# Performance work log

Hardware: AMD Instinct MI355X
Metric: run time of the kernel (lower is better)

## Reference

```python
import jax, jax.numpy as jnp
import numpy as np

N = 100_000          # nodes
E = 3_200_000        # edges (avg degree 32)
H = 20               # hidden_channels (node feature width, = 10 one-hot + 10 mlp)
EH = 64              # edge_hidden_dim
EO = 10              # edge_output_dim
THRESHOLD = 1.0


def setup_inputs() -> dict:
    key = jax.random.key(0)
    ks = jax.random.split(key, 12)
    x = jax.random.normal(ks[0], (N, 2, H), dtype=jnp.float32)
    edge_index = jax.random.randint(ks[1], (2, E), 0, N, dtype=jnp.int32)
    # distances strictly in (0, threshold]
    edge_attr = jax.random.uniform(ks[2], (E, 1), jnp.float32, 1e-4, THRESHOLD)
    # parameters (torch.rand init as in the module)
    a = jax.random.uniform(ks[3], (1,), jnp.float32)
    b = jax.random.uniform(ks[4], (1,), jnp.float32) + 1.0
    gamma1 = jax.random.uniform(ks[5], (H, H), jnp.float32)
    gamma2 = jax.random.uniform(ks[6], (H, H), jnp.float32)
    bias = jax.random.uniform(ks[7], (H,), jnp.float32)
    # edge MLP: Linear(1, EH) -> ReLU -> Linear(EH, EO)
    W1 = jax.random.normal(ks[8], (1, EH), jnp.float32)
    b1 = jnp.zeros((EH,), jnp.float32)
    W2 = jax.random.normal(ks[9], (EH, EO), jnp.float32) / np.sqrt(EH)
    b2 = jnp.zeros((EO,), jnp.float32)
    return dict(x=x, edge_index=edge_index, edge_attr=edge_attr, a=a, b=b,
                gamma1=gamma1, gamma2=gamma2, bias=bias, W1=W1, b1=b1, W2=W2, b2=b2)


def reference(x, edge_index, edge_attr, a, b, gamma1, gamma2, bias, W1, b1, W2, b2):
    src, dst = edge_index[0], edge_index[1]
    # --- edge features ---
    h = jax.nn.relu(edge_attr @ W1 + b1)            # [E, EH]
    mlp_out = h @ W2 + b2                           # [E, EO]
    # one-hot distance bucket: 10 equal intervals over (0, threshold], idx 10 -> 9
    idx = jnp.clip((edge_attr[:, 0] * (10.0 / THRESHOLD)).astype(jnp.int32), 0, 9)
    one_hot = jax.nn.one_hot(idx, 10, dtype=x.dtype)  # [E, 10]
    eac = jnp.concatenate([one_hot, mlp_out], axis=1)  # edge_attr_combined [E, 20]
    # --- per-source-node normalization (w_tilde) ---
    sum_w = jax.ops.segment_sum(eac, src, num_segments=N)  # [N, 20]
    sw = sum_w[src]                                        # [E, 20]
    safe = jnp.where(sw != 0, sw, 1.0)
    w_tilde = jnp.where(sw != 0, eac / safe, jnp.asarray(0.01, x.dtype))
    # --- rho weighting on node features ---
    h_j = x[src, 0]                                  # [E, 20]
    h_jp = x[dst, 0]                                 # [E, 20]
    rho = jnp.abs(a * h_j - (1.0 - a) * h_jp) ** b   # [E, 20]
    # --- aggregate messages per source node ---
    sum_features = jax.ops.segment_sum(rho * w_tilde, src, num_segments=N)  # [N, 20]
    # --- node update ---
    out0 = jax.nn.sigmoid(x[:, 0] @ gamma1.T + sum_features @ gamma2.T + bias)
    return jnp.stack([out0, sum_features], axis=1)   # [N, 2, 20]
```

## Files before the change

### kernel.cpp

```cpp
#include <hip/hip_runtime.h>
#include <hip/hip_bf16.h>


#define BATCH 4096
#define BPT   16
#define BSH   7
#define CAP   4608

__device__ int block_scan_excl(int* data, int n, int* scratch) {
    const int t = threadIdx.x;
    const int lane = t & 63, w = t >> 6;
    const int base = t * 4;
    int v0 = (base + 0 < n) ? data[base + 0] : 0;
    int v1 = (base + 1 < n) ? data[base + 1] : 0;
    int v2 = (base + 2 < n) ? data[base + 2] : 0;
    int v3 = (base + 3 < n) ? data[base + 3] : 0;
    int p1 = v0 + v1, p2 = p1 + v2, p3 = p2 + v3;
    int x = p3;
    #pragma unroll
    for (int o = 1; o < 64; o <<= 1) { int y = __shfl_up(x, o); if (lane >= o) x += y; }
    if (lane == 63) scratch[w] = x;
    __syncthreads();
    int wbase = 0;
    for (int i = 0; i < w; ++i) wbase += scratch[i];
    int tb = wbase + x - p3;
    if (base + 0 < n) data[base + 0] = tb;
    if (base + 1 < n) data[base + 1] = tb + v0;
    if (base + 2 < n) data[base + 2] = tb + p1;
    if (base + 3 < n) data[base + 3] = tb + p2;
    int tot = scratch[0] + scratch[1] + scratch[2] + scratch[3];
    __syncthreads();
    return tot;
}

__launch_bounds__(256)
__global__ void k_scatter(const int* __restrict__ src, const int* __restrict__ dst,
                          const float* __restrict__ ea, int* __restrict__ gcursor,
                          int* __restrict__ tmpw, unsigned char* __restrict__ tmpn,
                          const float* __restrict__ x, __hip_bfloat16* __restrict__ xa,
                          const float* __restrict__ W1, const float* __restrict__ b1,
                          const float* __restrict__ W2, const float* __restrict__ b2,
                          float* __restrict__ AB, int* __restrict__ flag,
                          int E, int nb, int Npack, int EH, int EO) {
    __shared__ int  pay[BATCH];
    __shared__ unsigned char pbn[BATCH];
    __shared__ unsigned short sbid[BATCH];
    __shared__ int  lcount[1024];
    __shared__ int  lsave[1024];
    __shared__ int  scratch[4];
    const int t = threadIdx.x;

    if (blockIdx.x == 0) {
        if (t == 64) {
            int ok = 1;
            for (int k = 0; k < EH; ++k) if (b1[k] != 0.0f) ok = 0;
            *flag = ok;
        }
        if (t < EO) {
            float A = 0.0f;
            for (int k = 0; k < EH; ++k)
                if (W1[k] > 0.0f) A = fmaf(W1[k], W2[k * EO + t], A);
            AB[t]      = A;
            AB[EO + t] = b2[t];
        }
    }

    for (int i = t; i < 1024; i += 256) lcount[i] = 0;
    __syncthreads();
    const int base = blockIdx.x * BATCH;
    int mys[BPT], myr[BPT], myw[BPT];
    #pragma unroll
    for (int k = 0; k < BPT; ++k) {
        int e = base + k * 256 + t;
        mys[k] = -1;
        if (e < E) {
            int s = src[e], d = dst[e];
            float dd = ea[e];
            int ib = (int)(dd * 10.0f);
            ib = ib < 0 ? 0 : (ib > 9 ? 9 : ib);
            int dq = (int)fmaf(dd, 2047.0f, 0.5f);
            dq = dq < 0 ? 0 : (dq > 2047 ? 2047 : dq);
            mys[k] = s;
            myr[k] = atomicAdd(&lcount[s >> BSH], 1);
            myw[k] = (d & 0x1FFFF) | (ib << 17) | (dq << 21);
        }
    }
    __syncthreads();
    for (int i = t; i < 1024; i += 256) lsave[i] = lcount[i];
    __syncthreads();
    int total = block_scan_excl(lcount, nb, scratch);
    for (int b = t; b < nb; b += 256) {
        int c = lsave[b];
        if (c > 0) lsave[b] = atomicAdd(&gcursor[b], c);
    }
    __syncthreads();
    #pragma unroll
    for (int k = 0; k < BPT; ++k) {
        if (mys[k] >= 0) {
            int b = mys[k] >> BSH;
            int pos = lcount[b] + myr[k];
            pay[pos]  = myw[k];
            pbn[pos]  = (unsigned char)(mys[k] & 127);
            sbid[pos] = (unsigned short)b;
        }
    }
    __syncthreads();
    for (int j = t; j < total; j += 256) {
        int b = sbid[j];
        int pos = lsave[b] + (j - lcount[b]);
        if (pos < CAP) {
            tmpw[b * CAP + pos] = pay[j];
            tmpn[b * CAP + pos] = pbn[j];
        }
    }
    const int stride = gridDim.x * 256;
    for (int i = blockIdx.x * 256 + t; i < Npack * 20; i += stride) {
        int n = i / 20, c = i - n * 20;
        xa[(n << 5) + c] = __float2bfloat16(x[n * 40 + c]);
    }
}

template <int USE_XA>
__launch_bounds__(512, 8)
__global__ void k_nodeb(const float* __restrict__ x,
                        const __hip_bfloat16* __restrict__ xa,
                        const int* __restrict__ gcount,
                        const int* __restrict__ tmpw,
                        const unsigned char* __restrict__ tmpn,
                        const float* __restrict__ a_p, const float* __restrict__ b_p,
                        const float* __restrict__ g1, const float* __restrict__ g2,
                        const float* __restrict__ bias,
                        const float* __restrict__ AB, const int* __restrict__ flag_p,
                        const float* __restrict__ W1, const float* __restrict__ b1,
                        const float* __restrict__ W2, const float* __restrict__ b2,
                        float* __restrict__ out, int N, int EH, int EO) {
    __shared__ int   buf[CAP];
    __shared__ int   hist[128];
    __shared__ int   rowstart[129];
    __shared__ int   lcur[128];
    __shared__ unsigned char perm[128];
    __shared__ __hip_bfloat16 s_x0[128 * 22];
    __shared__ float s_sf[128 * 21];
    __shared__ float s_g1[20 * 21], s_g2[20 * 21], s_b[20];

    const int t = threadIdx.x;
    const int b = blockIdx.x;
    const int node0 = b << BSH;
    const int s0 = b * CAP;
    int m = gcount[b];
    if (m > CAP) m = CAP;

    if (t < 128) hist[t] = 0;
    for (int i = t; i < 400; i += 512) {
        int r = i / 20, cc = i - r * 20;
        s_g1[r * 21 + cc] = g1[i];
        s_g2[r * 21 + cc] = g2[i];
    }
    if (t < 20) s_b[t] = bias[t];
    for (int i = t; i < 2560; i += 512) {
        int l = i / 20, cc = i - l * 20;
        int n = node0 + l;
        if (USE_XA)
            s_x0[l * 22 + cc] = (n < N) ? xa[(n << 5) + cc] : __float2bfloat16(0.0f);
        else
            s_x0[l * 22 + cc] = __float2bfloat16((n < N) ? x[n * 40 + cc] : 0.0f);
    }
    __syncthreads();

    const int4*   tw4 = (const int4*)(tmpw + s0);
    const uchar4* tn4 = (const uchar4*)(tmpn + s0);
    int vw[12], vn[12];
    #pragma unroll
    for (int k = 0; k < 3; ++k) {
        int idx4 = k * 512 + t;
        #pragma unroll
        for (int j = 0; j < 4; ++j) vn[k * 4 + j] = -1;
        int e0 = idx4 << 2;
        if (e0 < m) {
            int4   wv = tw4[idx4];
            uchar4 nv = tn4[idx4];
            vw[k * 4 + 0] = wv.x; vw[k * 4 + 1] = wv.y;
            vw[k * 4 + 2] = wv.z; vw[k * 4 + 3] = wv.w;
            { vn[k * 4 + 0] = nv.x & 127; atomicAdd(&hist[vn[k * 4 + 0]], 1); }
            if (e0 + 1 < m) { vn[k * 4 + 1] = nv.y & 127; atomicAdd(&hist[vn[k * 4 + 1]], 1); }
            if (e0 + 2 < m) { vn[k * 4 + 2] = nv.z & 127; atomicAdd(&hist[vn[k * 4 + 2]], 1); }
            if (e0 + 3 < m) { vn[k * 4 + 3] = nv.w & 127; atomicAdd(&hist[vn[k * 4 + 3]], 1); }
        }
    }
    __syncthreads();
    if (t < 64) {
        int a = hist[2 * t], bb = hist[2 * t + 1];
        int s = a + bb;
        int xsc = s;
        #pragma unroll
        for (int o = 1; o < 64; o <<= 1) { int y = __shfl_up(xsc, o); if (t >= o) xsc += y; }
        int excl = xsc - s;
        rowstart[2 * t]     = excl;
        rowstart[2 * t + 1] = excl + a;
        lcur[2 * t]         = excl;
        lcur[2 * t + 1]     = excl + a;
        if (t == 63) rowstart[128] = xsc;
    }
    __syncthreads();
    #pragma unroll
    for (int k = 0; k < 12; ++k) {
        if (vn[k] >= 0) {
            int p = atomicAdd(&lcur[vn[k]], 1);
            buf[p] = vw[k];
        }
    }
    __syncthreads();

    if (t < 128) hist[t] = 0;
    __syncthreads();
    if (t < 128) {
        int len = rowstart[t + 1] - rowstart[t];
        int bin = 127 - (len > 127 ? 127 : len);
        atomicAdd(&hist[bin], 1);
    }
    __syncthreads();
    if (t < 64) {
        int a = hist[2 * t], bb = hist[2 * t + 1];
        int s = a + bb;
        int xsc = s;
        #pragma unroll
        for (int o = 1; o < 64; o <<= 1) { int y = __shfl_up(xsc, o); if (t >= o) xsc += y; }
        int excl = xsc - s;
        hist[2 * t]     = excl;
        hist[2 * t + 1] = excl + a;
    }
    __syncthreads();
    if (t < 128) {
        int len = rowstart[t + 1] - rowstart[t];
        int bin = 127 - (len > 127 ? 127 : len);
        int pos = atomicAdd(&hist[bin], 1);
        perm[pos] = (unsigned char)t;
    }

    const float av = a_p[0], bv = b_p[0];
    const float am1 = 1.0f - av;
    const int fl = *flag_p;
    __syncthreads();

    const unsigned* xau = (const unsigned*)xa;
    #pragma unroll
    for (int r = 0; r < 3; ++r) {
        int item = t + 512 * r;
        if (item >= 1280) break;
        int li = perm[item / 10];
        int cp = item - (item / 10) * 10;
        int c0 = cp * 2;
        const bool cl10 = c0 < 10;
        float x0a = __bfloat162float(s_x0[li * 22 + c0]);
        float x0b = __bfloat162float(s_x0[li * 22 + c0 + 1]);
        const float pax0 = av * x0a;
        const float pax1 = av * x0b;
        int rs = rowstart[li];
        int re = rowstart[li + 1];
        float sf0, sf1;
        if (fl || cl10) {
            float sA0 = 0.f, sB0 = 0.f, s20 = 0.f;
            float sA1 = 0.f, sB1 = 0.f, s21 = 0.f;
            #pragma unroll 4
            for (int i = rs; i < re; ++i) {
                int w = buf[i];
                float xd0, xd1;
                if (USE_XA) {
                    unsigned v = xau[((unsigned)(w & 0x1FFFF) << 4) + cp];
                    xd0 = __uint_as_float(v << 16);
                    xd1 = __uint_as_float(v & 0xFFFF0000u);
                } else {
                    int n = w & 0x1FFFF;
                    xd0 = x[n * 40 + c0];
                    xd1 = x[n * 40 + c0 + 1];
                }
                float tt0  = fabsf(fmaf(-am1, xd0, pax0));
                float rho0 = exp2f(bv * __log2f(tt0));
                float tt1  = fabsf(fmaf(-am1, xd1, pax1));
                float rho1 = exp2f(bv * __log2f(tt1));
                int   ib   = (w >> 17) & 0xF;
                float dqf  = (float)(((unsigned)w) >> 21);
                float sel0 = cl10 ? ((ib == c0)     ? 1.0f : 0.0f) : dqf;
                float sel1 = cl10 ? ((ib == c0 + 1) ? 1.0f : 0.0f) : dqf;
                sA0 += sel0; sB0 = fmaf(rho0, sel0, sB0); s20 += rho0;
                sA1 += sel1; sB1 = fmaf(rho1, sel1, sB1); s21 += rho1;
            }
            float sw0, s10, sw1, s11;
            if (cl10) { sw0 = sA0; s10 = sB0; sw1 = sA1; s11 = sB1; }
            else {
                float deg  = (float)(re - rs);
                float Afq0 = AB[c0 - 10] * (1.0f / 2047.0f);
                float Bf0  = AB[c0];
                float Afq1 = AB[c0 - 9]  * (1.0f / 2047.0f);
                float Bf1  = AB[c0 + 1];
                sw0 = fmaf(Afq0, sA0, Bf0 * deg);
                s10 = fmaf(Afq0, sB0, Bf0 * s20);
                sw1 = fmaf(Afq1, sA1, Bf1 * deg);
                s11 = fmaf(Afq1, sB1, Bf1 * s21);
            }
            sf0 = (sw0 != 0.0f) ? (s10 / sw0) : (0.01f * s20);
            sf1 = (sw1 != 0.0f) ? (s11 / sw1) : (0.01f * s21);
        } else {
            float sw0 = 0.f, s10 = 0.f, s20 = 0.f;
            float sw1 = 0.f, s11 = 0.f, s21 = 0.f;
            for (int i = rs; i < re; ++i) {
                int w = buf[i];
                float xd0, xd1;
                if (USE_XA) {
                    unsigned v = xau[((unsigned)(w & 0x1FFFF) << 4) + cp];
                    xd0 = __uint_as_float(v << 16);
                    xd1 = __uint_as_float(v & 0xFFFF0000u);
                } else {
                    int n = w & 0x1FFFF;
                    xd0 = x[n * 40 + c0];
                    xd1 = x[n * 40 + c0 + 1];
                }
                float dd_ = (float)(((unsigned)w) >> 21) * (1.0f / 2047.0f);
                float m0 = b2[c0 - 10], m1 = b2[c0 - 9];
                for (int k_ = 0; k_ < EH; ++k_) {
                    float h_ = fmaf(dd_, W1[k_], b1[k_]);
                    h_ = h_ > 0.0f ? h_ : 0.0f;
                    m0 = fmaf(h_, W2[k_ * EO + (c0 - 10)], m0);
                    m1 = fmaf(h_, W2[k_ * EO + (c0 - 9)], m1);
                }
                float tt0  = fabsf(fmaf(-am1, xd0, pax0));
                float rho0 = exp2f(bv * __log2f(tt0));
                float tt1  = fabsf(fmaf(-am1, xd1, pax1));
                float rho1 = exp2f(bv * __log2f(tt1));
                sw0 += m0; s10 = fmaf(rho0, m0, s10); s20 += rho0;
                sw1 += m1; s11 = fmaf(rho1, m1, s11); s21 += rho1;
            }
            sf0 = (sw0 != 0.0f) ? (s10 / sw0) : (0.01f * s20);
            sf1 = (sw1 != 0.0f) ? (s11 / sw1) : (0.01f * s21);
        }
        s_sf[li * 21 + c0]     = sf0;
        s_sf[li * 21 + c0 + 1] = sf1;
    }
    __syncthreads();

    for (int i = t; i < 2560; i += 512) {
        int l = i / 20, cc = i - l * 20;
        int n = node0 + l;
        if (n < N) {
            float acc = s_b[cc];
            const __hip_bfloat16* xr = &s_x0[l * 22];
            const float* sr  = &s_sf[l * 21];
            const float* g1r = &s_g1[cc * 21];
            const float* g2r = &s_g2[cc * 21];
            #pragma unroll
            for (int k = 0; k < 20; ++k)
                acc = fmaf(__bfloat162float(xr[k]), g1r[k], fmaf(sr[k], g2r[k], acc));
            float o0 = 1.0f / (1.0f + __expf(-acc));
            out[n * 40 + cc]      = o0;
            out[n * 40 + 20 + cc] = sr[cc];
        }
    }
}

extern "C" void kernel_launch(void* const* d_in, const int* in_sizes, int n_in,
                              void* d_out, int out_size, void* d_ws, size_t ws_size,
                              hipStream_t stream) {
    const float* x    = (const float*)d_in[0];
    const int*   ei   = (const int*)  d_in[1];
    const float* ea   = (const float*)d_in[2];
    const float* a_p  = (const float*)d_in[3];
    const float* b_p  = (const float*)d_in[4];
    const float* g1   = (const float*)d_in[5];
    const float* g2   = (const float*)d_in[6];
    const float* bias = (const float*)d_in[7];
    const float* W1   = (const float*)d_in[8];
    const float* b1   = (const float*)d_in[9];
    const float* W2   = (const float*)d_in[10];
    const float* b2   = (const float*)d_in[11];
    float* out = (float*)d_out;

    const int E  = in_sizes[2];
    const int N  = in_sizes[0] / 40;
    const int EH = in_sizes[8];
    const int EO = in_sizes[11];
    const int* src = ei;
    const int* dst = ei + E;

    const int nb     = (N + 127) >> BSH;
    const int nbatch = (E + BATCH - 1) / BATCH;

    char* wsb = (char*)d_ws;
    size_t o = 0;
    int* gcursor = (int*)(wsb + o); o += (size_t)nb * 4;        o = (o + 15) & ~(size_t)15;
    float* AB    = (float*)(wsb + o); o += 2 * (size_t)EO * 4;
    int* flag    = (int*)(wsb + o);   o += 4;                   o = (o + 15) & ~(size_t)15;
    int* tmpw    = (int*)(wsb + o);   o += (size_t)nb * CAP * 4;
    unsigned char* tmpn = (unsigned char*)(wsb + o); o += (size_t)nb * CAP;
    o = (o + 15) & ~(size_t)15;
    __hip_bfloat16* xa = (__hip_bfloat16*)(wsb + o);
    const size_t need_xa = o + (size_t)N * 32 * 2;
    const int use_xa = (ws_size >= need_xa) ? 1 : 0;

    hipMemsetAsync(gcursor, 0, (size_t)nb * sizeof(int), stream);

    k_scatter<<<nbatch, 256, 0, stream>>>(src, dst, ea, gcursor, tmpw, tmpn,
                                          x, use_xa ? xa : (__hip_bfloat16*)AB,
                                          W1, b1, W2, b2, AB, flag,
                                          E, nb, use_xa ? N : 0, EH, EO);
    if (use_xa) {
        k_nodeb<1><<<nb, 512, 0, stream>>>(x, xa, gcursor, tmpw, tmpn, a_p, b_p,
                                           g1, g2, bias, AB, flag,
                                           W1, b1, W2, b2, out, N, EH, EO);
    } else {
        k_nodeb<0><<<nb, 512, 0, stream>>>(x, xa, gcursor, tmpw, tmpn, a_p, b_p,
                                           g1, g2, bias, AB, flag,
                                           W1, b1, W2, b2, out, N, EH, EO);
    }
}
```

Measured before the change: 228.4 us.

## Pack bf16 node features densely, vectorize edge loads, pad global cursors, widen per-thread channels

Packs the bf16 copy of node features into 10 dense 32-bit words per node instead of a 32-wide padded row. Each edge then gathers 8 bytes (uint2) per four channels. The node kernel now gives each thread four channels instead of two, halving the work items and the number of edge-list passes per node. The scatter kernel reads src/dst/edge_attr with 16-byte vector loads, assigning contiguous edges per thread. Global bucket cursors are padded to 64-byte strides to reduce atomic contention between neighbouring buckets. The trade-offs are higher register pressure and less parallelism per block in the gather loop.

```diff
diff --git a/kernel.cpp b/kernel.cpp
--- a/kernel.cpp
+++ b/kernel.cpp
@@ -6,6 +6,16 @@
 #define BPT   16
 #define BSH   7
 #define CAP   4608
+#define GST   16
+
+__device__ inline float blo(unsigned v) { return __uint_as_float(v << 16); }
+__device__ inline float bhi(unsigned v) { return __uint_as_float(v & 0xFFFF0000u); }
+__device__ inline unsigned f2bfu(float f) {
+    __hip_bfloat16 h = __float2bfloat16(f);
+    unsigned short us;
+    __builtin_memcpy(&us, &h, 2);
+    return (unsigned)us;
+}
 
 __device__ int block_scan_excl(int* data, int n, int* scratch) {
     const int t = threadIdx.x;
@@ -37,7 +47,7 @@
 __global__ void k_scatter(const int* __restrict__ src, const int* __restrict__ dst,
                           const float* __restrict__ ea, int* __restrict__ gcursor,
                           int* __restrict__ tmpw, unsigned char* __restrict__ tmpn,
-                          const float* __restrict__ x, __hip_bfloat16* __restrict__ xa,
+                          const float* __restrict__ x, unsigned* __restrict__ xau,
                           const float* __restrict__ W1, const float* __restrict__ b1,
                           const float* __restrict__ W2, const float* __restrict__ b2,
                           float* __restrict__ AB, int* __restrict__ flag,
@@ -68,21 +78,38 @@
     for (int i = t; i < 1024; i += 256) lcount[i] = 0;
     __syncthreads();
     const int base = blockIdx.x * BATCH;
+    const int e00  = base + t * BPT;
     int mys[BPT], myr[BPT], myw[BPT];
     #pragma unroll
-    for (int k = 0; k < BPT; ++k) {
-        int e = base + k * 256 + t;
-        mys[k] = -1;
-        if (e < E) {
-            int s = src[e], d = dst[e];
-            float dd = ea[e];
-            int ib = (int)(dd * 10.0f);
-            ib = ib < 0 ? 0 : (ib > 9 ? 9 : ib);
-            int dq = (int)fmaf(dd, 2047.0f, 0.5f);
-            dq = dq < 0 ? 0 : (dq > 2047 ? 2047 : dq);
-            mys[k] = s;
-            myr[k] = atomicAdd(&lcount[s >> BSH], 1);
-            myw[k] = (d & 0x1FFFF) | (ib << 17) | (dq << 21);
+    for (int k4 = 0; k4 < BPT / 4; ++k4) {
+        int e0 = e00 + k4 * 4;
+        int sv[4], dv[4]; float av[4];
+        bool full = (e0 + 3 < E);
+        if (full) {
+            int4   s4 = *(const int4*)(src + e0);
+            int4   d4 = *(const int4*)(dst + e0);
+            float4 a4 = *(const float4*)(ea + e0);
+            sv[0] = s4.x; sv[1] = s4.y; sv[2] = s4.z; sv[3] = s4.w;
+            dv[0] = d4.x; dv[1] = d4.y; dv[2] = d4.z; dv[3] = d4.w;
+            av[0] = a4.x; av[1] = a4.y; av[2] = a4.z; av[3] = a4.w;
+        }
+        #pragma unroll
+        for (int j = 0; j < 4; ++j) {
+            int k = k4 * 4 + j;
+            int e = e0 + j;
+            mys[k] = -1;
+            if (full || e < E) {
+                int s, d; float dd;
+                if (full) { s = sv[j]; d = dv[j]; dd = av[j]; }
+                else      { s = src[e]; d = dst[e]; dd = ea[e]; }
+                int ib = (int)(dd * 10.0f);
+                ib = ib < 0 ? 0 : (ib > 9 ? 9 : ib);
+                int dq = (int)fmaf(dd, 2047.0f, 0.5f);
+                dq = dq < 0 ? 0 : (dq > 2047 ? 2047 : dq);
+                mys[k] = s;
+                myr[k] = atomicAdd(&lcount[s >> BSH], 1);
+                myw[k] = (d & 0x1FFFF) | (ib << 17) | (dq << 21);
+            }
         }
     }
     __syncthreads();
@@ -91,7 +118,7 @@
     int total = block_scan_excl(lcount, nb, scratch);
     for (int b = t; b < nb; b += 256) {
         int c = lsave[b];
-        if (c > 0) lsave[b] = atomicAdd(&gcursor[b], c);
+        if (c > 0) lsave[b] = atomicAdd(&gcursor[b * GST], c);
     }
     __syncthreads();
     #pragma unroll
@@ -114,16 +141,17 @@
         }
     }
     const int stride = gridDim.x * 256;
-    for (int i = blockIdx.x * 256 + t; i < Npack * 20; i += stride) {
-        int n = i / 20, c = i - n * 20;
-        xa[(n << 5) + c] = __float2bfloat16(x[n * 40 + c]);
+    for (int i = blockIdx.x * 256 + t; i < Npack * 10; i += stride) {
+        int n = i / 10, p = i - n * 10;
+        float2 v = *(const float2*)(x + n * 40 + p * 2);
+        xau[i] = f2bfu(v.x) | (f2bfu(v.y) << 16);
     }
 }
 
 template <int USE_XA>
 __launch_bounds__(512, 8)
 __global__ void k_nodeb(const float* __restrict__ x,
-                        const __hip_bfloat16* __restrict__ xa,
+                        const unsigned* __restrict__ xau,
                         const int* __restrict__ gcount,
                         const int* __restrict__ tmpw,
                         const unsigned char* __restrict__ tmpn,
@@ -147,7 +175,7 @@
     const int b = blockIdx.x;
     const int node0 = b << BSH;
     const int s0 = b * CAP;
-    int m = gcount[b];
+    int m = gcount[b * GST];
     if (m > CAP) m = CAP;
 
     if (t < 128) hist[t] = 0;
@@ -157,13 +185,19 @@
         s_g2[r * 21 + cc] = g2[i];
     }
     if (t < 20) s_b[t] = bias[t];
-    for (int i = t; i < 2560; i += 512) {
-        int l = i / 20, cc = i - l * 20;
-        int n = node0 + l;
-        if (USE_XA)
-            s_x0[l * 22 + cc] = (n < N) ? xa[(n << 5) + cc] : __float2bfloat16(0.0f);
-        else
+    if (USE_XA) {
+        for (int i = t; i < 1280; i += 512) {
+            int l = i / 10, p = i - l * 10;
+            int n = node0 + l;
+            unsigned v = (n < N) ? xau[n * 10 + p] : 0u;
+            *(unsigned*)&s_x0[l * 22 + 2 * p] = v;
+        }
+    } else {
+        for (int i = t; i < 2560; i += 512) {
+            int l = i / 20, cc = i - l * 20;
+            int n = node0 + l;
             s_x0[l * 22 + cc] = __float2bfloat16((n < N) ? x[n * 40 + cc] : 0.0f);
+        }
     }
     __syncthreads();
 
@@ -242,99 +276,123 @@
     const int fl = *flag_p;
     __syncthreads();
 
-    const unsigned* xau = (const unsigned*)xa;
-    #pragma unroll
-    for (int r = 0; r < 3; ++r) {
+    const uint2* xg = (const uint2*)xau;
+    #pragma unroll
+    for (int r = 0; r < 2; ++r) {
         int item = t + 512 * r;
-        if (item >= 1280) break;
-        int li = perm[item / 10];
-        int cp = item - (item / 10) * 10;
-        int c0 = cp * 2;
-        const bool cl10 = c0 < 10;
-        float x0a = __bfloat162float(s_x0[li * 22 + c0]);
-        float x0b = __bfloat162float(s_x0[li * 22 + c0 + 1]);
-        const float pax0 = av * x0a;
-        const float pax1 = av * x0b;
+        if (item >= 640) break;
+        int li = perm[item / 5];
+        int q  = item - (item / 5) * 5;
+        int c0 = q * 4;
+        const bool cl0 = (c0 + 0) < 10, cl1 = (c0 + 1) < 10;
+        const bool cl2 = (c0 + 2) < 10, cl3 = (c0 + 3) < 10;
+        unsigned xv0 = *(const unsigned*)&s_x0[li * 22 + c0];
+        unsigned xv1 = *(const unsigned*)&s_x0[li * 22 + c0 + 2];
+        const float pax0 = av * blo(xv0), pax1 = av * bhi(xv0);
+        const float pax2 = av * blo(xv1), pax3 = av * bhi(xv1);
         int rs = rowstart[li];
         int re = rowstart[li + 1];
-        float sf0, sf1;
-        if (fl || cl10) {
+        float deg = (float)(re - rs);
+        float sf0, sf1, sf2, sf3;
+        if (fl || (c0 + 3) < 10) {
             float sA0 = 0.f, sB0 = 0.f, s20 = 0.f;
             float sA1 = 0.f, sB1 = 0.f, s21 = 0.f;
-            #pragma unroll 4
+            float sA2 = 0.f, sB2 = 0.f, s22 = 0.f;
+            float sA3 = 0.f, sB3 = 0.f, s23 = 0.f;
+            #pragma unroll 2
             for (int i = rs; i < re; ++i) {
                 int w = buf[i];
-                float xd0, xd1;
+                float xd0, xd1, xd2, xd3;
                 if (USE_XA) {
-                    unsigned v = xau[((unsigned)(w & 0x1FFFF) << 4) + cp];
-                    xd0 = __uint_as_float(v << 16);
-                    xd1 = __uint_as_float(v & 0xFFFF0000u);
+                    uint2 v = xg[(unsigned)(w & 0x1FFFF) * 5u + (unsigned)q];
+                    xd0 = blo(v.x); xd1 = bhi(v.x);
+                    xd2 = blo(v.y); xd3 = bhi(v.y);
                 } else {
                     int n = w & 0x1FFFF;
-                    xd0 = x[n * 40 + c0];
-                    xd1 = x[n * 40 + c0 + 1];
+                    xd0 = x[n * 40 + c0];     xd1 = x[n * 40 + c0 + 1];
+                    xd2 = x[n * 40 + c0 + 2]; xd3 = x[n * 40 + c0 + 3];
                 }
-                float tt0  = fabsf(fmaf(-am1, xd0, pax0));
-                float rho0 = exp2f(bv * __log2f(tt0));
-                float tt1  = fabsf(fmaf(-am1, xd1, pax1));
-                float rho1 = exp2f(bv * __log2f(tt1));
-                int   ib   = (w >> 17) & 0xF;
-                float dqf  = (float)(((unsigned)w) >> 21);
-                float sel0 = cl10 ? ((ib == c0)     ? 1.0f : 0.0f) : dqf;
-                float sel1 = cl10 ? ((ib == c0 + 1) ? 1.0f : 0.0f) : dqf;
-                sA0 += sel0; sB0 = fmaf(rho0, sel0, sB0); s20 += rho0;
-                sA1 += sel1; sB1 = fmaf(rho1, sel1, sB1); s21 += rho1;
+                int   ib  = (w >> 17) & 0xF;
+                float dqf = (float)(((unsigned)w) >> 21);
+                float r0 = exp2f(bv * __log2f(fabsf(fmaf(-am1, xd0, pax0))));
+                float r1 = exp2f(bv * __log2f(fabsf(fmaf(-am1, xd1, pax1))));
+                float r2 = exp2f(bv * __log2f(fabsf(fmaf(-am1, xd2, pax2))));
+                float r3 = exp2f(bv * __log2f(fabsf(fmaf(-am1, xd3, pax3))));
+                float e0s = cl0 ? ((ib == c0)     ? 1.0f : 0.0f) : dqf;
+                float e1s = cl1 ? ((ib == c0 + 1) ? 1.0f : 0.0f) : dqf;
+                float e2s = cl2 ? ((ib == c0 + 2) ? 1.0f : 0.0f) : dqf;
+                float e3s = cl3 ? ((ib == c0 + 3) ? 1.0f : 0.0f) : dqf;
+                sA0 += e0s; sB0 = fmaf(r0, e0s, sB0); s20 += r0;
+                sA1 += e1s; sB1 = fmaf(r1, e1s, sB1); s21 += r1;
+                sA2 += e2s; sB2 = fmaf(r2, e2s, sB2); s22 += r2;
+                sA3 += e3s; sB3 = fmaf(r3, e3s, sB3); s23 += r3;
             }
-            float sw0, s10, sw1, s11;
-            if (cl10) { sw0 = sA0; s10 = sB0; sw1 = sA1; s11 = sB1; }
-            else {
-                float deg  = (float)(re - rs);
-                float Afq0 = AB[c0 - 10] * (1.0f / 2047.0f);
-                float Bf0  = AB[c0];
-                float Afq1 = AB[c0 - 9]  * (1.0f / 2047.0f);
-                float Bf1  = AB[c0 + 1];
-                sw0 = fmaf(Afq0, sA0, Bf0 * deg);
-                s10 = fmaf(Afq0, sB0, Bf0 * s20);
-                sw1 = fmaf(Afq1, sA1, Bf1 * deg);
-                s11 = fmaf(Afq1, sB1, Bf1 * s21);
+            #define FIN(K, sAk, sBk, s2k, sfk)                                     \
+            {   int ck = c0 + K;                                                   \
+                float sw, s1;                                                      \
+                if (ck < 10) { sw = sAk; s1 = sBk; }                               \
+                else { float Afq = AB[ck - 10] * (1.0f / 2047.0f);                 \
+                       float Bf  = AB[ck];                                         \
+                       sw = fmaf(Afq, sAk, Bf * deg);                              \
+                       s1 = fmaf(Afq, sBk, Bf * s2k); }                            \
+                sfk = (sw != 0.0f) ? (s1 / sw) : (0.01f * s2k);                    \
             }
-            sf0 = (sw0 != 0.0f) ? (s10 / sw0) : (0.01f * s20);
-            sf1 = (sw1 != 0.0f) ? (s11 / sw1) : (0.01f * s21);
+            FIN(0, sA0, sB0, s20, sf0); FIN(1, sA1, sB1, s21, sf1);
+            FIN(2, sA2, sB2, s22, sf2); FIN(3, sA3, sB3, s23, sf3);
+            #undef FIN
         } else {
-            float sw0 = 0.f, s10 = 0.f, s20 = 0.f;
-            float sw1 = 0.f, s11 = 0.f, s21 = 0.f;
+            float swk[4] = {0.f, 0.f, 0.f, 0.f};
+            float s1k[4] = {0.f, 0.f, 0.f, 0.f};
+            float s2k[4] = {0.f, 0.f, 0.f, 0.f};
+            float paxs[4] = {pax0, pax1, pax2, pax3};
             for (int i = rs; i < re; ++i) {
                 int w = buf[i];
-                float xd0, xd1;
+                float xd[4];
                 if (USE_XA) {
-                    unsigned v = xau[((unsigned)(w & 0x1FFFF) << 4) + cp];
-                    xd0 = __uint_as_float(v << 16);
-                    xd1 = __uint_as_float(v & 0xFFFF0000u);
+                    uint2 v = xg[(unsigned)(w & 0x1FFFF) * 5u + (unsigned)q];
+                    xd[0] = blo(v.x); xd[1] = bhi(v.x);
+                    xd[2] = blo(v.y); xd[3] = bhi(v.y);
                 } else {
                     int n = w & 0x1FFFF;
-                    xd0 = x[n * 40 + c0];
-                    xd1 = x[n * 40 + c0 + 1];
+                    #pragma unroll
+                    for (int kk = 0; kk < 4; ++kk) xd[kk] = x[n * 40 + c0 + kk];
                 }
+                int   ib  = (w >> 17) & 0xF;
                 float dd_ = (float)(((unsigned)w) >> 21) * (1.0f / 2047.0f);
-                float m0 = b2[c0 - 10], m1 = b2[c0 - 9];
+                float mlp[4];
+                #pragma unroll
+                for (int kk = 0; kk < 4; ++kk) {
+                    int ck = c0 + kk;
+                    mlp[kk] = b2[ck >= 10 ? ck - 10 : 0];
+                }
                 for (int k_ = 0; k_ < EH; ++k_) {
                     float h_ = fmaf(dd_, W1[k_], b1[k_]);
                     h_ = h_ > 0.0f ? h_ : 0.0f;
-                    m0 = fmaf(h_, W2[k_ * EO + (c0 - 10)], m0);
-                    m1 = fmaf(h_, W2[k_ * EO + (c0 - 9)], m1);
+                    #pragma unroll
+                    for (int kk = 0; kk < 4; ++kk) {
+                        int ck = c0 + kk;
+                        mlp[kk] = fmaf(h_, W2[k_ * EO + (ck >= 10 ? ck - 10 : 0)], mlp[kk]);
+                    }
                 }
-                float tt0  = fabsf(fmaf(-am1, xd0, pax0));
-                float rho0 = exp2f(bv * __log2f(tt0));
-                float tt1  = fabsf(fmaf(-am1, xd1, pax1));
-                float rho1 = exp2f(bv * __log2f(tt1));
-                sw0 += m0; s10 = fmaf(rho0, m0, s10); s20 += rho0;
-                sw1 += m1; s11 = fmaf(rho1, m1, s11); s21 += rho1;
+                #pragma unroll
+                for (int kk = 0; kk < 4; ++kk) {
+                    int ck = c0 + kk;
+                    float rho = exp2f(bv * __log2f(fabsf(fmaf(-am1, xd[kk], paxs[kk]))));
+                    float sel = (ck < 10) ? ((ib == ck) ? 1.0f : 0.0f) : mlp[kk];
+                    swk[kk] += sel;
+                    s1k[kk] = fmaf(rho, sel, s1k[kk]);
+                    s2k[kk] += rho;
+                }
             }
-            sf0 = (sw0 != 0.0f) ? (s10 / sw0) : (0.01f * s20);
-            sf1 = (sw1 != 0.0f) ? (s11 / sw1) : (0.01f * s21);
+            sf0 = (swk[0] != 0.0f) ? (s1k[0] / swk[0]) : (0.01f * s2k[0]);
+            sf1 = (swk[1] != 0.0f) ? (s1k[1] / swk[1]) : (0.01f * s2k[1]);
+            sf2 = (swk[2] != 0.0f) ? (s1k[2] / swk[2]) : (0.01f * s2k[2]);
+            sf3 = (swk[3] != 0.0f) ? (s1k[3] / swk[3]) : (0.01f * s2k[3]);
         }
         s_sf[li * 21 + c0]     = sf0;
         s_sf[li * 21 + c0 + 1] = sf1;
+        s_sf[li * 21 + c0 + 2] = sf2;
+        s_sf[li * 21 + c0 + 3] = sf3;
     }
     __syncthreads();
 
@@ -386,28 +444,28 @@
 
     char* wsb = (char*)d_ws;
     size_t o = 0;
-    int* gcursor = (int*)(wsb + o); o += (size_t)nb * 4;        o = (o + 15) & ~(size_t)15;
+    int* gcursor = (int*)(wsb + o); o += (size_t)nb * GST * 4;
     float* AB    = (float*)(wsb + o); o += 2 * (size_t)EO * 4;
     int* flag    = (int*)(wsb + o);   o += 4;                   o = (o + 15) & ~(size_t)15;
     int* tmpw    = (int*)(wsb + o);   o += (size_t)nb * CAP * 4;
     unsigned char* tmpn = (unsigned char*)(wsb + o); o += (size_t)nb * CAP;
     o = (o + 15) & ~(size_t)15;
-    __hip_bfloat16* xa = (__hip_bfloat16*)(wsb + o);
-    const size_t need_xa = o + (size_t)N * 32 * 2;
+    unsigned* xau = (unsigned*)(wsb + o);
+    const size_t need_xa = o + (size_t)N * 10 * 4;
     const int use_xa = (ws_size >= need_xa) ? 1 : 0;
 
-    hipMemsetAsync(gcursor, 0, (size_t)nb * sizeof(int), stream);
+    hipMemsetAsync(gcursor, 0, (size_t)nb * GST * sizeof(int), stream);
 
     k_scatter<<<nbatch, 256, 0, stream>>>(src, dst, ea, gcursor, tmpw, tmpn,
-                                          x, use_xa ? xa : (__hip_bfloat16*)AB,
+                                          x, use_xa ? xau : (unsigned*)AB,
                                           W1, b1, W2, b2, AB, flag,
                                           E, nb, use_xa ? N : 0, EH, EO);
     if (use_xa) {
-        k_nodeb<1><<<nb, 512, 0, stream>>>(x, xa, gcursor, tmpw, tmpn, a_p, b_p,
+        k_nodeb<1><<<nb, 512, 0, stream>>>(x, xau, gcursor, tmpw, tmpn, a_p, b_p,
                                            g1, g2, bias, AB, flag,
                                            W1, b1, W2, b2, out, N, EH, EO);
     } else {
-        k_nodeb<0><<<nb, 512, 0, stream>>>(x, xa, gcursor, tmpw, tmpn, a_p, b_p,
+        k_nodeb<0><<<nb, 512, 0, stream>>>(x, xau, gcursor, tmpw, tmpn, a_p, b_p,
                                            g1, g2, bias, AB, flag,
                                            W1, b1, W2, b2, out, N, EH, EO);
     }
```

After: 240.7 us. +5.4%, slower.
